# Optimization experiments

Hardware: AMD Instinct MI355X
Metric: run time of the kernel (lower is better)

The kernel has to match this reference:

```python
import jax, jax.numpy as jnp
import numpy as np

SUBSTEPS = 2  # fixed RK4 substeps per save interval (replaces adaptive diffrax solver)


def setup_inputs() -> dict:
    key = jax.random.key(0)
    k = jax.random.split(key, 6)
    dim, hidden, neighbors, T = 512, 2048, 512, 9
    ts = jnp.linspace(0.0, 1.0, T, dtype=jnp.float32)
    y0 = jax.random.normal(k[0], (dim,), dtype=jnp.float32)
    Dy0 = jax.random.normal(k[1], (neighbors, dim), dtype=jnp.float32) * 0.01
    W1 = jax.random.normal(k[2], (dim, hidden), dtype=jnp.float32) / np.sqrt(dim).astype(np.float32)
    b1 = jax.random.normal(k[3], (hidden,), dtype=jnp.float32) * 0.01
    W2 = jax.random.normal(k[4], (hidden, dim), dtype=jnp.float32) / np.sqrt(hidden).astype(np.float32)
    b2 = jax.random.normal(k[5], (dim,), dtype=jnp.float32) * 0.01
    return {"ts": ts, "y0": y0, "Dy0": Dy0, "W1": W1, "b1": b1, "W2": W2, "b2": b2}


def reference(ts, y0, Dy0, W1, b1, W2, b2):
    tmap = jax.tree_util.tree_map

    def f(y):  # autonomous NeuralODE vector field: 2-layer tanh MLP
        return jnp.tanh(y @ W1 + b1) @ W2 + b2

    def rhs(u):
        y, Dy = u                      # y: [dim], Dy: [neighbors, dim]
        z = y + Dy                     # [neighbors, dim]

        def second_order(z_):          # per-neighbor, z_: [dim]
            def first_order(y_):
                return jax.jvp(f, (y_,), (z_ - y_,))
            (dy, dDy1), (_, dDy2) = jax.jvp(first_order, (y,), (z_ - y,))
            return dy, 1.5 * dDy1 + 0.5 * dDy2

        dy, dDy = jax.vmap(second_order, out_axes=(None, 0))(z)
        return (dy, dDy)

    def axpy(u, k, c):
        return tmap(lambda a, b: a + c * b, u, k)

    def rk4(u, dt):
        k1 = rhs(u)
        k2 = rhs(axpy(u, k1, dt * 0.5))
        k3 = rhs(axpy(u, k2, dt * 0.5))
        k4 = rhs(axpy(u, k3, dt))
        return tmap(lambda a, a1, a2, a3, a4: a + (dt / 6.0) * (a1 + 2.0 * a2 + 2.0 * a3 + a4),
                    u, k1, k2, k3, k4)

    def interval(u, tpair):
        t0, t1 = tpair
        dt = (t1 - t0) / SUBSTEPS
        def body(u_, _):
            return rk4(u_, dt), None
        u_new, _ = jax.lax.scan(body, u, None, length=SUBSTEPS)
        return u_new, u_new

    u0 = (y0, Dy0)
    _, (ys, Dys) = jax.lax.scan(interval, u0, (ts[:-1], ts[1:]))
    ys = jnp.concatenate([y0[None], ys], axis=0)        # [T, dim]
    Dys = jnp.concatenate([Dy0[None], Dys], axis=0)     # [T, neighbors, dim]
    # pack (y, Dy) trajectories into one array: [T, 1+neighbors, dim]
    return jnp.concatenate([ys[:, None, :], Dys], axis=1)
```

## Files before the change

kernel.cpp:

```cpp
#include <hip/hip_runtime.h>
#include <hip/hip_bf16.h>

typedef __attribute__((ext_vector_type(8))) short short8;
typedef float f32x4 __attribute__((ext_vector_type(4)));

#define DIM 512
#define HID 2048
#define ROWSZ (513*512)
#define DT 0.0625f

#define WAITV(n) asm volatile("s_waitcnt vmcnt(" #n ")" ::: "memory")
#define SBAR()   asm volatile("s_barrier" ::: "memory")
typedef const __attribute__((address_space(1))) void* gas1;
typedef __attribute__((address_space(3))) void* las3;
#define GLL16(g,l,aux) __builtin_amdgcn_global_load_lds((gas1)(g),(las3)(l),16,0,aux)
#define GLL4(g,l,aux)  __builtin_amdgcn_global_load_lds((gas1)(g),(las3)(l),4,0,aux)

__device__ __forceinline__ float bf2f(unsigned short s){ return __uint_as_float(((unsigned)s)<<16); }
__device__ __forceinline__ unsigned short f2bfu(float f){ __hip_bfloat16 h=__float2bfloat16(f); return *(unsigned short*)&h; }
__device__ __forceinline__ float dot8(uint4 wq, const float* a){
  const unsigned short* ws=(const unsigned short*)&wq;
  float s=0.f;
#pragma unroll
  for(int i=0;i<8;++i) s += bf2f(ws[i])*a[i];
  return s;
}
__device__ __forceinline__ float dot8bb(uint4 wq, const unsigned short* a){
  const unsigned short* ws=(const unsigned short*)&wq;
  float s=0.f;
#pragma unroll
  for(int i=0;i<8;++i) s += bf2f(ws[i])*bf2f(a[i]);
  return s;
}

__device__ __forceinline__ void xbar(int* arr, int* gen, int target, bool lead){
  asm volatile("s_waitcnt vmcnt(0) lgkmcnt(0)" ::: "memory");
  __syncthreads();
  if (threadIdx.x == 0){
    __hip_atomic_fetch_add(arr, 1, __ATOMIC_RELAXED, __HIP_MEMORY_SCOPE_AGENT);
    if (lead){
      while (__hip_atomic_load(arr, __ATOMIC_RELAXED, __HIP_MEMORY_SCOPE_AGENT) < 32*target)
        __builtin_amdgcn_s_sleep(2);
      __hip_atomic_store(gen, target, __ATOMIC_RELAXED, __HIP_MEMORY_SCOPE_AGENT);
    } else {
      while (__hip_atomic_load(gen, __ATOMIC_RELAXED, __HIP_MEMORY_SCOPE_AGENT) < target)
        __builtin_amdgcn_s_sleep(4);
    }
  }
  __syncthreads();
}

__device__ __forceinline__ void post_flag(int* f, int seq){
  asm volatile("s_waitcnt vmcnt(0) lgkmcnt(0)" ::: "memory");
  __syncthreads();
  if (threadIdx.x == 0)
    __hip_atomic_store(f, seq, __ATOMIC_RELAXED, __HIP_MEMORY_SCOPE_AGENT);
}
__device__ __forceinline__ void wait_flags32(int* base, int seq){
  if (threadIdx.x < 32){
    while (__hip_atomic_load(&base[threadIdx.x], __ATOMIC_RELAXED, __HIP_MEMORY_SCOPE_AGENT) < seq)
      __builtin_amdgcn_s_sleep(2);
  }
  __syncthreads();
}

__global__ void k_transpose_bf16(const float* __restrict__ src,
                                 __hip_bfloat16* __restrict__ dst, int R, int C) {
  __shared__ float tile[32][33];
  int c0 = blockIdx.x * 32, r0 = blockIdx.y * 32;
  int tx = threadIdx.x & 31, ty = threadIdx.x >> 5;
  for (int i = 0; i < 32; i += 8)
    tile[ty + i][tx] = src[(size_t)(r0 + ty + i) * C + c0 + tx];
  __syncthreads();
  for (int i = 0; i < 32; i += 8)
    dst[(size_t)(c0 + ty + i) * R + r0 + tx] = __float2bfloat16(tile[tx][ty + i]);
}

__global__ __launch_bounds__(512, 1) void k_persist(
    const float* __restrict__ y0, const float* __restrict__ Dy0,
    const unsigned short* __restrict__ W1t, const unsigned short* __restrict__ W2t,
    const float* __restrict__ b1, const float* __restrict__ b2,
    unsigned short* __restrict__ Vbuf, unsigned short* __restrict__ tbuf,
    float* __restrict__ yts, unsigned short* __restrict__ a_ss, float* __restrict__ pbuf,
    int* __restrict__ ctrl, float* __restrict__ out) {
  __shared__ __align__(16) short W1L[64 * 512];
  __shared__ __align__(16) short W2L[32 * 1024];
  __shared__ __align__(16) short ring[3][4096];
  __shared__ float ytL[DIM];
  __shared__ __align__(16) unsigned short asL[1024];
  __shared__ float pacc[512];
  __shared__ float c1L[64], c2L[64];
  __shared__ int bcast[2];

  const int t = threadIdx.x;
  if (t == 0) {
    int x;
    asm volatile("s_getreg_b32 %0, hwreg(HW_REG_XCC_ID)" : "=s"(x));
    x &= 7;
    bcast[0] = x;
    bcast[1] = atomicAdd(&ctrl[x], 1);
  }
  __syncthreads();
  const int xcd = bcast[0];
  const int sl  = bcast[1] & 31;
  const bool lead = (sl == 0);
  int* arr = ctrl + 64 + xcd * 64;
  int* gen = arr + 32;
  int* flgAb = ctrl + 704 + xcd * 32;
  int* flgBb = ctrl + 960 + xcd * 32;

  const int w = t >> 6, lane = t & 63, quad = lane >> 4, l16 = lane & 15;
  const int r8 = lane >> 3;
  const int mX = xcd * 64;
  const int nA = sl * 64;
  const int ni = sl >> 1, kq = sl & 1;
  const int nB = ni * 32;
  const int kb = kq * 1024;
  float* ytx = yts + xcd * DIM;
  unsigned short* asx = a_ss + xcd * HID;
  float* rec = pbuf + (size_t)(xcd * 16 + ni) * 2112;
  int* flg = ctrl + 576 + xcd * 16 + ni;

  const int awm = (w & 1) * 32, awn = (w >> 1) * 16;
  const int bwm = (w >> 1) * 16, bwn = (w & 1) * 16;

  f32x4 DyR = {0.f,0.f,0.f,0.f}, K1 = DyR, K2 = DyR, K3 = DyR;
  float yR = 0.f, kd1 = 0.f, kd2 = 0.f, kd3 = 0.f;
  const int erow0 = mX + bwm + quad * 4;
  const int ecol  = nB + bwn + l16;

  auto issueA = [&](int buf, int c) {
    int k0 = c * 64;
    GLL16(Vbuf + (size_t)(mX + w * 8 + r8) * DIM + k0 + (((lane & 7) ^ r8) << 3),
          &ring[buf][(w * 8) * 64], 1);
  };
  auto issueB = [&](int buf, int c) {
    int k0 = kb + c * 64;
    GLL16(tbuf + (size_t)(mX + w * 8 + r8) * HID + k0 + (((lane & 7) ^ r8) << 3),
          &ring[buf][(w * 8) * 64], 1);
  };

#pragma unroll
  for (int i = 0; i < 8; ++i) {
    int r = w * 8 + i;
    int src = ((lane & ~7) | ((lane & 7) ^ (r & 7))) << 3;
    GLL16(W1t + (size_t)(nA + r) * DIM + src, &W1L[r * 512], 0);
  }
#pragma unroll
  for (int i = 0; i < 4; ++i) {
    int r = w * 4 + i;
#pragma unroll
    for (int h2 = 0; h2 < 2; ++h2) {
      int g0 = h2 * 64 + lane;
      int src = ((g0 & ~7) | ((g0 & 7) ^ (r & 7))) << 3;
      GLL16(W2t + (size_t)(nB + r) * HID + kb + src, &W2L[r * 1024 + h2 * 512], 0);
    }
  }
  if (kq == 0) {
#pragma unroll
    for (int r = 0; r < 4; ++r) {
      float v = Dy0[(size_t)(erow0 + r) * DIM + ecol];
      DyR[r] = v;
      Vbuf[(size_t)(erow0 + r) * DIM + ecol] = f2bfu(v);
      out[DIM + (size_t)(erow0 + r) * DIM + ecol] = v;
    }
    if (t < 32) {
      float v = y0[nB + t];
      yR = v;
      ytx[nB + t] = v;
      if (xcd == 0) out[nB + t] = v;
    }
  }
  WAITV(0);
  __syncthreads();
  xbar(arr, gen, 1, lead);

  for (int ss = 0; ss < 16; ++ss) {
    for (int st = 0; st < 4; ++st) {
      const float cn = (st == 2) ? DT : 0.5f * DT;
      const int seq = ss * 4 + st + 1;
      {
        wait_flags32(flgBb, seq - 1);
        GLL4(ytx + w * 64 + lane, &ytL[w * 64], 1);
        issueA(0, 0); issueA(1, 1);
        WAITV(2); SBAR();
        {
          int row = t & 63, seg = t >> 6;
          float hs = 0.f;
#pragma unroll
          for (int g = 0; g < 8; ++g) {
            int lg = seg * 8 + g;
            int ps = ((lg & ~7) | ((lg & 7) ^ (row & 7))) << 3;
            hs += dot8(*(const uint4*)&W1L[row * 512 + ps], &ytL[lg * 8]);
          }
          pacc[seg * 64 + row] = hs;
        }
        __syncthreads();
        if (t < 64) {
          float hsum = b1[nA + t];
#pragma unroll
          for (int q = 0; q < 8; ++q) hsum += pacc[q * 64 + t];
          float a = tanhf(hsum);
          float ap = 1.f - a * a;
          c1L[t] = ap; c2L[t] = -a * ap;
          asx[nA + t] = f2bfu(a);
        }
        f32x4 acc0 = {0.f,0.f,0.f,0.f}, acc1 = acc0;
#pragma unroll
        for (int c = 0; c < 8; ++c) {
          if (c < 7) { WAITV(1); } else { WAITV(0); }
          SBAR();
          if (c < 6) issueA((c + 2) % 3, c + 2);
          const short* tA = ring[c % 3];
#pragma unroll
          for (int kk = 0; kk < 64; kk += 32) {
            int lg = (kk >> 3) + quad;
            int pa0 = awm + l16, pa1 = awm + 16 + l16, pb = awn + l16;
            short8 a0 = *(const short8*)&tA[pa0 * 64 + ((lg ^ (pa0 & 7)) << 3)];
            short8 a1 = *(const short8*)&tA[pa1 * 64 + ((lg ^ (pa1 & 7)) << 3)];
            int gb = c * 8 + lg;
            short8 b = *(const short8*)&W1L[pb * 512 + (((gb & ~7) | ((gb & 7) ^ (pb & 7))) << 3)];
            acc0 = __builtin_amdgcn_mfma_f32_16x16x32_bf16(a0, b, acc0, 0, 0, 0);
            acc1 = __builtin_amdgcn_mfma_f32_16x16x32_bf16(a1, b, acc1, 0, 0, 0);
          }
        }
        int row0 = mX + awm + quad * 4;
        int coln = nA + awn + l16;
        float C1 = c1L[awn + l16], C2 = c2L[awn + l16];
#pragma unroll
        for (int r = 0; r < 4; ++r) {
          float g0 = acc0[r], g1 = acc1[r];
          tbuf[(size_t)(row0 + r) * HID + coln]      = f2bfu(g0 * (C1 + C2 * g0));
          tbuf[(size_t)(row0 + 16 + r) * HID + coln] = f2bfu(g1 * (C1 + C2 * g1));
        }
        post_flag(&flgAb[sl], seq);
      }
      {
        wait_flags32(flgAb, seq);
        GLL4((const unsigned short*)asx + kb + w * 128 + lane * 2, &asL[w * 128], 1);
        issueB(0, 0); issueB(1, 1);
        WAITV(2); SBAR();
        {
          int row = t & 31, seg = t >> 5;
          float ds = 0.f;
#pragma unroll
          for (int g = 0; g < 8; ++g) {
            int lg = seg * 8 + g;
            int ps = ((lg & ~7) | ((lg & 7) ^ (row & 7))) << 3;
            ds += dot8bb(*(const uint4*)&W2L[row * 1024 + ps], &asL[lg * 8]);
          }
          pacc[seg * 32 + row] = ds;
        }
        __syncthreads();
        float dyown = 0.f;
        if (t < 32) {
#pragma unroll
          for (int q = 0; q < 16; ++q) dyown += pacc[q * 32 + t];
        }
        f32x4 acc = {0.f,0.f,0.f,0.f};
#pragma unroll
        for (int c = 0; c < 16; ++c) {
          if (c < 15) { WAITV(1); } else { WAITV(0); }
          SBAR();
          if (c < 14) issueB((c + 2) % 3, c + 2);
          const short* tA = ring[c % 3];
#pragma unroll
          for (int kk = 0; kk < 64; kk += 32) {
            int lg = (kk >> 3) + quad;
            int pa = bwm + l16, pb = bwn + l16;
            short8 a = *(const short8*)&tA[pa * 64 + ((lg ^ (pa & 7)) << 3)];
            int gb = c * 8 + lg;
            short8 b = *(const short8*)&W2L[pb * 1024 + (((gb & ~7) | ((gb & 7) ^ (pb & 7))) << 3)];
            acc = __builtin_amdgcn_mfma_f32_16x16x32_bf16(a, b, acc, 0, 0, 0);
          }
        }
        if (kq == 1) {
          int lrow = bwm + quad * 4, lcol = bwn + l16;
#pragma unroll
          for (int r = 0; r < 4; ++r) rec[(lrow + r) * 32 + lcol] = acc[r];
          if (t < 32) rec[2048 + t] = dyown;
          asm volatile("s_waitcnt vmcnt(0)" ::: "memory");
          __syncthreads();
          if (t == 0) {
            __hip_atomic_store(flg, seq, __ATOMIC_RELAXED, __HIP_MEMORY_SCOPE_AGENT);
            __hip_atomic_store(&flgBb[sl], seq, __ATOMIC_RELAXED, __HIP_MEMORY_SCOPE_AGENT);
          }
        } else {
          if (t == 0) {
            while (__hip_atomic_load(flg, __ATOMIC_RELAXED, __HIP_MEMORY_SCOPE_AGENT) < seq)
              __builtin_amdgcn_s_sleep(1);
          }
          __syncthreads();
          float* pLDS = (float*)&ring[0][0];
          GLL16(rec + w * 256 + lane * 4, pLDS + w * 256, 1);
          if (w == 0) GLL4(rec + 2048 + lane, pLDS + 2048, 1);
          WAITV(0);
          __syncthreads();
          int lrow = bwm + quad * 4, lcol = bwn + l16;
          f32x4 o = acc;
#pragma unroll
          for (int r = 0; r < 4; ++r) o[r] += pLDS[(lrow + r) * 32 + lcol];
          if (st == 0) K1 = o; else if (st == 1) K2 = o; else if (st == 2) K3 = o;
          if (st < 3) {
#pragma unroll
            for (int r = 0; r < 4; ++r) {
              float v = DyR[r] + cn * o[r];
              Vbuf[(size_t)(erow0 + r) * DIM + ecol] = f2bfu(v);
            }
          } else {
            const float dt6 = DT / 6.f;
#pragma unroll
            for (int r = 0; r < 4; ++r) {
              float v = DyR[r] + dt6 * (K1[r] + 2.f * K2[r] + 2.f * K3[r] + o[r]);
              DyR[r] = v;
              Vbuf[(size_t)(erow0 + r) * DIM + ecol] = f2bfu(v);
              if (ss & 1) out[(size_t)(ss / 2 + 1) * ROWSZ + DIM + (size_t)(erow0 + r) * DIM + ecol] = v;
            }
          }
          if (t < 32) {
            float k4 = dyown + pLDS[2048 + t] + b2[nB + t];
            if (st == 0) kd1 = k4; else if (st == 1) kd2 = k4; else if (st == 2) kd3 = k4;
            if (st < 3) {
              ytx[nB + t] = yR + cn * k4;
            } else {
              yR += (DT / 6.f) * (kd1 + 2.f * kd2 + 2.f * kd3 + k4);
              ytx[nB + t] = yR;
              if ((ss & 1) && xcd == 0) out[(size_t)(ss / 2 + 1) * ROWSZ + nB + t] = yR;
            }
          }
          post_flag(&flgBb[sl], seq);
        }
      }
    }
  }
}

extern "C" void kernel_launch(void* const* d_in, const int* in_sizes, int n_in,
                              void* d_out, int out_size, void* d_ws, size_t ws_size,
                              hipStream_t stream) {
  const float* y0  = (const float*)d_in[1];
  const float* Dy0 = (const float*)d_in[2];
  const float* W1  = (const float*)d_in[3];
  const float* b1  = (const float*)d_in[4];
  const float* W2  = (const float*)d_in[5];
  const float* b2  = (const float*)d_in[6];
  float* out = (float*)d_out;

  char* p = (char*)d_ws;
  auto alloc = [&](size_t bytes) {
    char* r = p;
    p += (bytes + 255) & ~(size_t)255;
    return r;
  };
  unsigned short* W1t  = (unsigned short*)alloc((size_t)HID * DIM * 2);
  unsigned short* W2t  = (unsigned short*)alloc((size_t)DIM * HID * 2);
  unsigned short* Vbuf = (unsigned short*)alloc((size_t)DIM * DIM * 2);
  unsigned short* tbuf = (unsigned short*)alloc((size_t)DIM * HID * 2);
  float* yts  = (float*)alloc(8 * DIM * 4);
  unsigned short* a_ss = (unsigned short*)alloc(8 * HID * 2);
  float* pbuf = (float*)alloc((size_t)8 * 16 * 2112 * 4);
  int* ctrl   = (int*)alloc(8192);

  hipMemsetAsync(ctrl, 0, 8192, stream);
  k_transpose_bf16<<<dim3(HID / 32, DIM / 32), 256, 0, stream>>>(W1, (__hip_bfloat16*)W1t, DIM, HID);
  k_transpose_bf16<<<dim3(DIM / 32, HID / 32), 256, 0, stream>>>(W2, (__hip_bfloat16*)W2t, HID, DIM);
  k_persist<<<256, 512, 0, stream>>>(y0, Dy0, W1t, W2t, b1, b2,
                                     Vbuf, tbuf, yts, a_ss, pbuf, ctrl, out);
}
```

Measured before the change: 808.5 us.

## Stream W1 tiles through a deeper unified LDS ring and overlap matvecs with MFMA

W1 is no longer held resident in LDS. Its 64-column tiles are streamed from global memory alongside the V tiles through a 5-deep unified ring, and the y·W1 matvec is folded into the MFMA loop. The second GEMM gets an 8-deep prefetch of t tiles, with the W2·a matvec interleaved into its chunk loop. The flag wait now covers only the 16 producer slices that share this block's K-half. The goal is to cut serial prologue phases and barrier stalls and to hide memory latency. In exchange, W1 is re-read from global (or L2) every stage, which adds memory traffic.

```diff
diff --git a/kernel.cpp b/kernel.cpp
--- a/kernel.cpp
+++ b/kernel.cpp
@@ -63,6 +63,13 @@
   }
   __syncthreads();
 }
+__device__ __forceinline__ void wait_flags16(int* base, int seq){
+  if (threadIdx.x < 16){
+    while (__hip_atomic_load(&base[threadIdx.x], __ATOMIC_RELAXED, __HIP_MEMORY_SCOPE_AGENT) < seq)
+      __builtin_amdgcn_s_sleep(2);
+  }
+  __syncthreads();
+}
 
 __global__ void k_transpose_bf16(const float* __restrict__ src,
                                  __hip_bfloat16* __restrict__ dst, int R, int C) {
@@ -83,9 +90,8 @@
     unsigned short* __restrict__ Vbuf, unsigned short* __restrict__ tbuf,
     float* __restrict__ yts, unsigned short* __restrict__ a_ss, float* __restrict__ pbuf,
     int* __restrict__ ctrl, float* __restrict__ out) {
-  __shared__ __align__(16) short W1L[64 * 512];
   __shared__ __align__(16) short W2L[32 * 1024];
-  __shared__ __align__(16) short ring[3][4096];
+  __shared__ __align__(16) short ringU[40960];
   __shared__ float ytL[DIM];
   __shared__ __align__(16) unsigned short asL[1024];
   __shared__ float pacc[512];
@@ -129,23 +135,19 @@
   const int erow0 = mX + bwm + quad * 4;
   const int ecol  = nB + bwn + l16;
 
-  auto issueA = [&](int buf, int c) {
-    int k0 = c * 64;
-    GLL16(Vbuf + (size_t)(mX + w * 8 + r8) * DIM + k0 + (((lane & 7) ^ r8) << 3),
-          &ring[buf][(w * 8) * 64], 1);
+  auto issueAV = [&](int p, int c) {
+    GLL16(Vbuf + (size_t)(mX + w * 8 + r8) * DIM + c * 64 + (((lane & 7) ^ r8) << 3),
+          &ringU[p * 8192 + (w * 8) * 64], 1);
   };
-  auto issueB = [&](int buf, int c) {
-    int k0 = kb + c * 64;
-    GLL16(tbuf + (size_t)(mX + w * 8 + r8) * HID + k0 + (((lane & 7) ^ r8) << 3),
-          &ring[buf][(w * 8) * 64], 1);
+  auto issueAW = [&](int p, int c) {
+    GLL16(W1t + (size_t)(nA + w * 8 + r8) * DIM + c * 64 + (((lane & 7) ^ r8) << 3),
+          &ringU[p * 8192 + 4096 + (w * 8) * 64], 0);
   };
-
-#pragma unroll
-  for (int i = 0; i < 8; ++i) {
-    int r = w * 8 + i;
-    int src = ((lane & ~7) | ((lane & 7) ^ (r & 7))) << 3;
-    GLL16(W1t + (size_t)(nA + r) * DIM + src, &W1L[r * 512], 0);
-  }
+  auto issueB = [&](int b, int c) {
+    GLL16(tbuf + (size_t)(mX + w * 8 + r8) * HID + kb + c * 64 + (((lane & 7) ^ r8) << 3),
+          &ringU[b * 4096 + (w * 8) * 64], 1);
+  };
+
 #pragma unroll
   for (int i = 0; i < 4; ++i) {
     int r = w * 4 + i;
@@ -182,19 +184,32 @@
       {
         wait_flags32(flgBb, seq - 1);
         GLL4(ytx + w * 64 + lane, &ytL[w * 64], 1);
-        issueA(0, 0); issueA(1, 1);
-        WAITV(2); SBAR();
-        {
-          int row = t & 63, seg = t >> 6;
-          float hs = 0.f;
-#pragma unroll
-          for (int g = 0; g < 8; ++g) {
-            int lg = seg * 8 + g;
-            int ps = ((lg & ~7) | ((lg & 7) ^ (row & 7))) << 3;
-            hs += dot8(*(const uint4*)&W1L[row * 512 + ps], &ytL[lg * 8]);
-          }
-          pacc[seg * 64 + row] = hs;
-        }
+        issueAV(0, 0); issueAW(0, 0);
+        issueAV(1, 1); issueAW(1, 1);
+        issueAV(2, 2); issueAW(2, 2);
+        float hs = 0.f;
+        f32x4 acc0 = {0.f,0.f,0.f,0.f}, acc1 = acc0;
+#pragma unroll
+        for (int c = 0; c < 8; ++c) {
+          if (c < 6) { WAITV(4); } else if (c == 6) { WAITV(2); } else { WAITV(0); }
+          SBAR();
+          if (c < 5) { int p = (c + 3) % 5; issueAV(p, c + 3); issueAW(p, c + 3); }
+          const short* tV = &ringU[(c % 5) * 8192];
+          const short* tW = tV + 4096;
+          hs += dot8(*(const uint4*)&tW[lane * 64 + ((w ^ (lane & 7)) << 3)],
+                     &ytL[c * 64 + w * 8]);
+#pragma unroll
+          for (int kk = 0; kk < 64; kk += 32) {
+            int lg = (kk >> 3) + quad;
+            int pa0 = awm + l16, pa1 = awm + 16 + l16, pbW = awn + l16;
+            short8 a0 = *(const short8*)&tV[pa0 * 64 + ((lg ^ (pa0 & 7)) << 3)];
+            short8 a1 = *(const short8*)&tV[pa1 * 64 + ((lg ^ (pa1 & 7)) << 3)];
+            short8 b  = *(const short8*)&tW[pbW * 64 + ((lg ^ (pbW & 7)) << 3)];
+            acc0 = __builtin_amdgcn_mfma_f32_16x16x32_bf16(a0, b, acc0, 0, 0, 0);
+            acc1 = __builtin_amdgcn_mfma_f32_16x16x32_bf16(a1, b, acc1, 0, 0, 0);
+          }
+        }
+        pacc[w * 64 + lane] = hs;
         __syncthreads();
         if (t < 64) {
           float hsum = b1[nA + t];
@@ -205,25 +220,7 @@
           c1L[t] = ap; c2L[t] = -a * ap;
           asx[nA + t] = f2bfu(a);
         }
-        f32x4 acc0 = {0.f,0.f,0.f,0.f}, acc1 = acc0;
-#pragma unroll
-        for (int c = 0; c < 8; ++c) {
-          if (c < 7) { WAITV(1); } else { WAITV(0); }
-          SBAR();
-          if (c < 6) issueA((c + 2) % 3, c + 2);
-          const short* tA = ring[c % 3];
-#pragma unroll
-          for (int kk = 0; kk < 64; kk += 32) {
-            int lg = (kk >> 3) + quad;
-            int pa0 = awm + l16, pa1 = awm + 16 + l16, pb = awn + l16;
-            short8 a0 = *(const short8*)&tA[pa0 * 64 + ((lg ^ (pa0 & 7)) << 3)];
-            short8 a1 = *(const short8*)&tA[pa1 * 64 + ((lg ^ (pa1 & 7)) << 3)];
-            int gb = c * 8 + lg;
-            short8 b = *(const short8*)&W1L[pb * 512 + (((gb & ~7) | ((gb & 7) ^ (pb & 7))) << 3)];
-            acc0 = __builtin_amdgcn_mfma_f32_16x16x32_bf16(a0, b, acc0, 0, 0, 0);
-            acc1 = __builtin_amdgcn_mfma_f32_16x16x32_bf16(a1, b, acc1, 0, 0, 0);
-          }
-        }
+        __syncthreads();
         int row0 = mX + awm + quad * 4;
         int coln = nA + awn + l16;
         float C1 = c1L[awn + l16], C2 = c2L[awn + l16];
@@ -236,34 +233,33 @@
         post_flag(&flgAb[sl], seq);
       }
       {
-        wait_flags32(flgAb, seq);
+        wait_flags16(flgAb + kq * 16, seq);
         GLL4((const unsigned short*)asx + kb + w * 128 + lane * 2, &asL[w * 128], 1);
-        issueB(0, 0); issueB(1, 1);
-        WAITV(2); SBAR();
-        {
-          int row = t & 31, seg = t >> 5;
-          float ds = 0.f;
-#pragma unroll
-          for (int g = 0; g < 8; ++g) {
-            int lg = seg * 8 + g;
-            int ps = ((lg & ~7) | ((lg & 7) ^ (row & 7))) << 3;
-            ds += dot8bb(*(const uint4*)&W2L[row * 1024 + ps], &asL[lg * 8]);
-          }
-          pacc[seg * 32 + row] = ds;
-        }
-        __syncthreads();
-        float dyown = 0.f;
-        if (t < 32) {
-#pragma unroll
-          for (int q = 0; q < 16; ++q) dyown += pacc[q * 32 + t];
-        }
+        issueB(0, 0); issueB(1, 1); issueB(2, 2); issueB(3, 3);
+        issueB(4, 4); issueB(5, 5); issueB(6, 6); issueB(7, 7);
+        float ds = 0.f;
+        const int drow = lane & 31;
+        const int dseg = t >> 5;
+        const int dslot = dseg & 7, dpar = dseg >> 3;
         f32x4 acc = {0.f,0.f,0.f,0.f};
 #pragma unroll
         for (int c = 0; c < 16; ++c) {
-          if (c < 15) { WAITV(1); } else { WAITV(0); }
+          if (c <= 8) { WAITV(7); }
+          else if (c == 9)  { WAITV(6); }
+          else if (c == 10) { WAITV(5); }
+          else if (c == 11) { WAITV(4); }
+          else if (c == 12) { WAITV(3); }
+          else if (c == 13) { WAITV(2); }
+          else if (c == 14) { WAITV(1); }
+          else { WAITV(0); }
           SBAR();
-          if (c < 14) issueB((c + 2) % 3, c + 2);
-          const short* tA = ring[c % 3];
+          if (c < 8) issueB((c + 8) % 10, c + 8);
+          const short* tA = &ringU[(c % 10) * 4096];
+          if ((c & 1) == dpar) {
+            int lg = c * 8 + dslot;
+            int ps = ((lg & ~7) | ((lg & 7) ^ (drow & 7))) << 3;
+            ds += dot8bb(*(const uint4*)&W2L[drow * 1024 + ps], &asL[lg * 8]);
+          }
 #pragma unroll
           for (int kk = 0; kk < 64; kk += 32) {
             int lg = (kk >> 3) + quad;
@@ -274,6 +270,13 @@
             acc = __builtin_amdgcn_mfma_f32_16x16x32_bf16(a, b, acc, 0, 0, 0);
           }
         }
+        pacc[dseg * 32 + drow] = ds;
+        __syncthreads();
+        float dyown = 0.f;
+        if (t < 32) {
+#pragma unroll
+          for (int q = 0; q < 16; ++q) dyown += pacc[q * 32 + t];
+        }
         if (kq == 1) {
           int lrow = bwm + quad * 4, lcol = bwn + l16;
 #pragma unroll
@@ -291,7 +294,7 @@
               __builtin_amdgcn_s_sleep(1);
           }
           __syncthreads();
-          float* pLDS = (float*)&ring[0][0];
+          float* pLDS = (float*)&ringU[0];
           GLL16(rec + w * 256 + lane * 4, pLDS + w * 256, 1);
           if (w == 0) GLL4(rec + 2048 + lane, pLDS + 2048, 1);
           WAITV(0);
```

New measurement: 827.8 us. 1.02x slower.

## Register double-buffer MFMA operands and narrow phase-B flag wait to needed producers

Applied to the files above, without the earlier changes.

The two MFMA K-loops now prefetch the next chunk's A and B fragments from LDS into a second register set, so those LDS reads overlap the current MFMAs. The global-to-LDS ring issue is moved ahead of the barrier, and waits are split into explicit vmcnt and lgkmcnt waits. Phase B now waits only on the 16 phase-A flags covering its own K half instead of all 32, which should shorten the cross-block synchronization stall. The trade-off is higher VGPR use, and the ring-slot reuse ordering needs care to avoid races.

```diff
diff --git a/kernel.cpp b/kernel.cpp
--- a/kernel.cpp
+++ b/kernel.cpp
@@ -10,6 +10,7 @@
 #define DT 0.0625f
 
 #define WAITV(n) asm volatile("s_waitcnt vmcnt(" #n ")" ::: "memory")
+#define WAITL()  asm volatile("s_waitcnt lgkmcnt(0)" ::: "memory")
 #define SBAR()   asm volatile("s_barrier" ::: "memory")
 typedef const __attribute__((address_space(1))) void* gas1;
 typedef __attribute__((address_space(3))) void* las3;
@@ -58,6 +59,13 @@
 }
 __device__ __forceinline__ void wait_flags32(int* base, int seq){
   if (threadIdx.x < 32){
+    while (__hip_atomic_load(&base[threadIdx.x], __ATOMIC_RELAXED, __HIP_MEMORY_SCOPE_AGENT) < seq)
+      __builtin_amdgcn_s_sleep(2);
+  }
+  __syncthreads();
+}
+__device__ __forceinline__ void wait_flags16(int* base, int seq){
+  if (threadIdx.x < 16){
     while (__hip_atomic_load(&base[threadIdx.x], __ATOMIC_RELAXED, __HIP_MEMORY_SCOPE_AGENT) < seq)
       __builtin_amdgcn_s_sleep(2);
   }
@@ -195,7 +203,7 @@
           }
           pacc[seg * 64 + row] = hs;
         }
-        __syncthreads();
+        WAITL(); SBAR();
         if (t < 64) {
           float hsum = b1[nA + t];
 #pragma unroll
@@ -206,23 +214,44 @@
           asx[nA + t] = f2bfu(a);
         }
         f32x4 acc0 = {0.f,0.f,0.f,0.f}, acc1 = acc0;
+        short8 ra0[2][2], ra1[2][2], rb[2][2];
+        const int pa0 = awm + l16, pa1 = awm + 16 + l16, pbW = awn + l16;
+        WAITV(1); SBAR();
+        {
+          const short* tA = ring[0];
+#pragma unroll
+          for (int k2 = 0; k2 < 2; ++k2) {
+            int lg = k2 * 4 + quad;
+            ra0[0][k2] = *(const short8*)&tA[pa0 * 64 + ((lg ^ (pa0 & 7)) << 3)];
+            ra1[0][k2] = *(const short8*)&tA[pa1 * 64 + ((lg ^ (pa1 & 7)) << 3)];
+            int gb = lg;
+            rb[0][k2] = *(const short8*)&W1L[pbW * 512 + (((gb & ~7) | ((gb & 7) ^ (pbW & 7))) << 3)];
+          }
+        }
+        WAITL();
 #pragma unroll
         for (int c = 0; c < 8; ++c) {
-          if (c < 7) { WAITV(1); } else { WAITV(0); }
-          SBAR();
-          if (c < 6) issueA((c + 2) % 3, c + 2);
-          const short* tA = ring[c % 3];
-#pragma unroll
-          for (int kk = 0; kk < 64; kk += 32) {
-            int lg = (kk >> 3) + quad;
-            int pa0 = awm + l16, pa1 = awm + 16 + l16, pb = awn + l16;
-            short8 a0 = *(const short8*)&tA[pa0 * 64 + ((lg ^ (pa0 & 7)) << 3)];
-            short8 a1 = *(const short8*)&tA[pa1 * 64 + ((lg ^ (pa1 & 7)) << 3)];
-            int gb = c * 8 + lg;
-            short8 b = *(const short8*)&W1L[pb * 512 + (((gb & ~7) | ((gb & 7) ^ (pb & 7))) << 3)];
-            acc0 = __builtin_amdgcn_mfma_f32_16x16x32_bf16(a0, b, acc0, 0, 0, 0);
-            acc1 = __builtin_amdgcn_mfma_f32_16x16x32_bf16(a1, b, acc1, 0, 0, 0);
-          }
+          const int pr = c & 1, nx = pr ^ 1;
+          if (c < 6)       { issueA((c + 2) % 3, c + 2); WAITV(1); }
+          else if (c == 6) { WAITV(0); }
+          if (c < 7) {
+            SBAR();
+            const short* tA = ring[(c + 1) % 3];
+#pragma unroll
+            for (int k2 = 0; k2 < 2; ++k2) {
+              int lg = k2 * 4 + quad;
+              ra0[nx][k2] = *(const short8*)&tA[pa0 * 64 + ((lg ^ (pa0 & 7)) << 3)];
+              ra1[nx][k2] = *(const short8*)&tA[pa1 * 64 + ((lg ^ (pa1 & 7)) << 3)];
+              int gb = (c + 1) * 8 + lg;
+              rb[nx][k2] = *(const short8*)&W1L[pbW * 512 + (((gb & ~7) | ((gb & 7) ^ (pbW & 7))) << 3)];
+            }
+          }
+#pragma unroll
+          for (int k2 = 0; k2 < 2; ++k2) {
+            acc0 = __builtin_amdgcn_mfma_f32_16x16x32_bf16(ra0[pr][k2], rb[pr][k2], acc0, 0, 0, 0);
+            acc1 = __builtin_amdgcn_mfma_f32_16x16x32_bf16(ra1[pr][k2], rb[pr][k2], acc1, 0, 0, 0);
+          }
+          if (c < 7) WAITL();
         }
         int row0 = mX + awm + quad * 4;
         int coln = nA + awn + l16;
@@ -236,7 +265,7 @@
         post_flag(&flgAb[sl], seq);
       }
       {
-        wait_flags32(flgAb, seq);
+        wait_flags16(flgAb + kq * 16, seq);
         GLL4((const unsigned short*)asx + kb + w * 128 + lane * 2, &asL[w * 128], 1);
         issueB(0, 0); issueB(1, 1);
         WAITV(2); SBAR();
@@ -251,28 +280,47 @@
           }
           pacc[seg * 32 + row] = ds;
         }
-        __syncthreads();
+        WAITL(); SBAR();
         float dyown = 0.f;
         if (t < 32) {
 #pragma unroll
           for (int q = 0; q < 16; ++q) dyown += pacc[q * 32 + t];
         }
         f32x4 acc = {0.f,0.f,0.f,0.f};
+        short8 rba[2][2], rbw[2][2];
+        const int paB = bwm + l16, pbB = bwn + l16;
+        WAITV(1); SBAR();
+        {
+          const short* tA = ring[0];
+#pragma unroll
+          for (int k2 = 0; k2 < 2; ++k2) {
+            int lg = k2 * 4 + quad;
+            rba[0][k2] = *(const short8*)&tA[paB * 64 + ((lg ^ (paB & 7)) << 3)];
+            int gb = lg;
+            rbw[0][k2] = *(const short8*)&W2L[pbB * 1024 + (((gb & ~7) | ((gb & 7) ^ (pbB & 7))) << 3)];
+          }
+        }
+        WAITL();
 #pragma unroll
         for (int c = 0; c < 16; ++c) {
-          if (c < 15) { WAITV(1); } else { WAITV(0); }
-          SBAR();
-          if (c < 14) issueB((c + 2) % 3, c + 2);
-          const short* tA = ring[c % 3];
-#pragma unroll
-          for (int kk = 0; kk < 64; kk += 32) {
-            int lg = (kk >> 3) + quad;
-            int pa = bwm + l16, pb = bwn + l16;
-            short8 a = *(const short8*)&tA[pa * 64 + ((lg ^ (pa & 7)) << 3)];
-            int gb = c * 8 + lg;
-            short8 b = *(const short8*)&W2L[pb * 1024 + (((gb & ~7) | ((gb & 7) ^ (pb & 7))) << 3)];
-            acc = __builtin_amdgcn_mfma_f32_16x16x32_bf16(a, b, acc, 0, 0, 0);
-          }
+          const int pr = c & 1, nx = pr ^ 1;
+          if (c < 14)       { issueB((c + 2) % 3, c + 2); WAITV(1); }
+          else if (c == 14) { WAITV(0); }
+          if (c < 15) {
+            SBAR();
+            const short* tA = ring[(c + 1) % 3];
+#pragma unroll
+            for (int k2 = 0; k2 < 2; ++k2) {
+              int lg = k2 * 4 + quad;
+              rba[nx][k2] = *(const short8*)&tA[paB * 64 + ((lg ^ (paB & 7)) << 3)];
+              int gb = (c + 1) * 8 + lg;
+              rbw[nx][k2] = *(const short8*)&W2L[pbB * 1024 + (((gb & ~7) | ((gb & 7) ^ (pbB & 7))) << 3)];
+            }
+          }
+#pragma unroll
+          for (int k2 = 0; k2 < 2; ++k2)
+            acc = __builtin_amdgcn_mfma_f32_16x16x32_bf16(rba[pr][k2], rbw[pr][k2], acc, 0, 0, 0);
+          if (c < 15) WAITL();
         }
         if (kq == 1) {
           int lrow = bwm + quad * 4, lcol = bwn + l16;
```

After: 802.0 us. About the same (-0.8%).
